# Kernel optimization log

Measured on AMD Instinct MI355X. Metric: run time of the kernel, lower is better.

Reference implementation:

```python
import jax, jax.numpy as jnp
import numpy as np

ATT_H = 256
DEC_H = 512
CTX = 1024  # 2 * encoder_hidden_size


def setup_inputs() -> dict:
    key = jax.random.key(0)
    ks = jax.random.split(key, 8)
    B, T = 32, 4096
    prev = jax.random.normal(ks[0], (B, 1, DEC_H), dtype=jnp.float32)
    enc = jax.random.normal(ks[1], (B, T, CTX), dtype=jnp.float32)
    # nn.Linear params: weight [out,in], bias [out]
    W_w = jax.random.normal(ks[2], (ATT_H, DEC_H), dtype=jnp.float32) / np.sqrt(DEC_H)
    W_b = jax.random.normal(ks[3], (ATT_H,), dtype=jnp.float32) * 0.01
    U_w = jax.random.normal(ks[4], (ATT_H, CTX), dtype=jnp.float32) / np.sqrt(CTX)
    U_b = jax.random.normal(ks[5], (ATT_H,), dtype=jnp.float32) * 0.01
    v = jax.random.uniform(ks[6], (ATT_H,), dtype=jnp.float32)
    return {
        "batch_size": B,
        "max_seq_len": T,
        "previous_decoder_hidden_state": prev,
        "encoder_final_hidden_layers": enc,
        "W_w": W_w, "W_b": W_b, "U_w": U_w, "U_b": U_b, "v": v,
    }


def reference(batch_size, max_seq_len, previous_decoder_hidden_state,
              encoder_final_hidden_layers, W_w, W_b, U_w, U_b, v):
    # tmp_1: [B,1,H] = W(prev); tmp_3: [B,T,H] = U(enc)
    tmp1 = jnp.einsum('bod,hd->boh', previous_decoder_hidden_state, W_w) + W_b
    tmp3 = jnp.einsum('btc,hc->bth', encoder_final_hidden_layers, U_w) + U_b
    # energy: [B,T] = relu(tmp1 + tmp3) . v
    energy = jnp.einsum('bth,h->bt', jax.nn.relu(tmp1 + tmp3), v)
    alpha = jax.nn.softmax(energy, axis=1)  # [B,T]
    # weighted sum over time -> context [B, 2E]
    c = jnp.einsum('bt,btc->bc', alpha, encoder_final_hidden_layers)
    return c
```

## Files before the change

kernel.cpp:

```cpp
#include <hip/hip_runtime.h>
#include <hip/hip_bf16.h>

#define BB   32
#define TT   4096
#define CTXD 1024
#define HH   256
#define DH   512
#define BT   64
#define NTILES (TT/BT)
#define BK   64
#define LDA  72

typedef __attribute__((ext_vector_type(8))) short bf16x8;
typedef __attribute__((ext_vector_type(4))) float f32x4;

static __device__ __forceinline__ unsigned short f2bf(float f) {
    unsigned int u = __float_as_uint(f);
    u += 0x7FFF + ((u >> 16) & 1);
    return (unsigned short)(u >> 16);
}

__global__ void uconv_kernel(const float* __restrict__ Uw, unsigned short* __restrict__ Ub) {
    int idx = blockIdx.x * blockDim.x + threadIdx.x;
    float4 u4 = ((const float4*)Uw)[idx];
    ushort4 o;
    o.x = f2bf(u4.x); o.y = f2bf(u4.y); o.z = f2bf(u4.z); o.w = f2bf(u4.w);
    ((ushort4*)Ub)[idx] = o;
}

__global__ void bias_kernel(const float* __restrict__ prev, const float* __restrict__ Ww,
                            const float* __restrict__ Wb, const float* __restrict__ Ubias,
                            float* __restrict__ bias) {
    __shared__ float ps[DH];
    int b = blockIdx.x, h = threadIdx.x;
    if (h < DH / 4) ((float4*)ps)[h] = ((const float4*)(prev + (size_t)b * DH))[h];
    __syncthreads();
    float acc = Wb[h] + Ubias[h];
    const float4* wr = (const float4*)(Ww + (size_t)h * DH);
    #pragma unroll 4
    for (int d = 0; d < DH / 4; ++d) {
        float4 w4 = wr[d];
        float4 p4 = ((const float4*)ps)[d];
        acc += w4.x * p4.x + w4.y * p4.y + w4.z * p4.z + w4.w * p4.w;
    }
    bias[b * HH + h] = acc;
}

__global__ void attn_main(const float* __restrict__ enc, const unsigned short* __restrict__ Ub,
                          const float* __restrict__ bias, const float* __restrict__ v,
                          float* __restrict__ partO, float* __restrict__ partM,
                          float* __restrict__ partL) {
    __shared__ __align__(16) unsigned short As[BT * LDA];
    __shared__ __align__(16) unsigned short Us[HH * LDA];
    __shared__ float epart[4][BT];
    __shared__ float pbuf[BT];

    const int tid  = threadIdx.x;
    const int lane = tid & 63;
    const int w    = tid >> 6;
    const int quad = lane >> 4;
    const int l15  = lane & 15;
    const int b    = blockIdx.x & 31;
    const int tile = blockIdx.x >> 5;
    const int t0   = tile * BT;
    const int pi   = b * NTILES + tile;

    const float* encBase = enc + ((size_t)b * TT + t0) * CTXD;

    f32x4 acc[4][4];
    #pragma unroll
    for (int mi = 0; mi < 4; ++mi)
        #pragma unroll
        for (int ni = 0; ni < 4; ++ni) acc[mi][ni] = (f32x4){0.f, 0.f, 0.f, 0.f};

    const int arow = tid >> 4;
    const int acg  = tid & 15;

    for (int kt = 0; kt < CTXD / BK; ++kt) {
        const float* ga = encBase + kt * BK;
        #pragma unroll
        for (int rr = 0; rr < 4; ++rr) {
            int row = arow + rr * 16;
            float4 a4 = *(const float4*)(ga + (size_t)row * CTXD + acg * 4);
            ushort4 o;
            o.x = f2bf(a4.x); o.y = f2bf(a4.y); o.z = f2bf(a4.z); o.w = f2bf(a4.w);
            *(ushort4*)&As[row * LDA + acg * 4] = o;
        }
        #pragma unroll
        for (int ii = 0; ii < 8; ++ii) {
            int idx = ii * 256 + tid;
            int row = idx >> 3;
            int g   = idx & 7;
            uint4 u = *(const uint4*)(Ub + (size_t)row * CTXD + kt * BK + g * 8);
            *(uint4*)&Us[row * LDA + g * 8] = u;
        }
        __syncthreads();
        #pragma unroll
        for (int ks = 0; ks < BK / 32; ++ks) {
            bf16x8 af[4], bfr[4];
            #pragma unroll
            for (int mi = 0; mi < 4; ++mi)
                af[mi] = *(const bf16x8*)&As[(mi * 16 + l15) * LDA + ks * 32 + quad * 8];
            #pragma unroll
            for (int ni = 0; ni < 4; ++ni)
                bfr[ni] = *(const bf16x8*)&Us[(w * 64 + ni * 16 + l15) * LDA + ks * 32 + quad * 8];
            #pragma unroll
            for (int mi = 0; mi < 4; ++mi)
                #pragma unroll
                for (int ni = 0; ni < 4; ++ni)
                    acc[mi][ni] = __builtin_amdgcn_mfma_f32_16x16x32_bf16(af[mi], bfr[ni], acc[mi][ni], 0, 0, 0);
        }
        __syncthreads();
    }

    float vv[4], bb[4];
    #pragma unroll
    for (int ni = 0; ni < 4; ++ni) {
        int h = w * 64 + ni * 16 + l15;
        vv[ni] = v[h];
        bb[ni] = bias[b * HH + h];
    }
    #pragma unroll
    for (int mi = 0; mi < 4; ++mi) {
        #pragma unroll
        for (int r = 0; r < 4; ++r) {
            float e = 0.f;
            #pragma unroll
            for (int ni = 0; ni < 4; ++ni) {
                float x = acc[mi][ni][r] + bb[ni];
                e += fmaxf(x, 0.f) * vv[ni];
            }
            e += __shfl_xor(e, 1);
            e += __shfl_xor(e, 2);
            e += __shfl_xor(e, 4);
            e += __shfl_xor(e, 8);
            if (l15 == 0) epart[w][mi * 16 + quad * 4 + r] = e;
        }
    }
    __syncthreads();

    if (tid < 64) {
        float e = epart[0][tid] + epart[1][tid] + epart[2][tid] + epart[3][tid];
        float m = e;
        #pragma unroll
        for (int off = 32; off; off >>= 1) m = fmaxf(m, __shfl_xor(m, off));
        float p = __expf(e - m);
        float l = p;
        #pragma unroll
        for (int off = 32; off; off >>= 1) l += __shfl_xor(l, off);
        pbuf[tid] = p;
        if (tid == 0) { partM[pi] = m; partL[pi] = l; }
    }
    __syncthreads();

    float4 o4 = {0.f, 0.f, 0.f, 0.f};
    #pragma unroll 4
    for (int t = 0; t < BT; ++t) {
        float p = pbuf[t];
        float4 ev = *(const float4*)(encBase + (size_t)t * CTXD + tid * 4);
        o4.x += p * ev.x; o4.y += p * ev.y; o4.z += p * ev.z; o4.w += p * ev.w;
    }
    *(float4*)(partO + (size_t)pi * CTXD + tid * 4) = o4;
}

__global__ void combine_kernel(const float* __restrict__ partO, const float* __restrict__ partM,
                               const float* __restrict__ partL, float* __restrict__ out) {
    __shared__ float sc[NTILES];
    __shared__ float sL;
    int b = blockIdx.x, tid = threadIdx.x;
    if (tid < 64) {
        float m = partM[b * NTILES + tid];
        float l = partL[b * NTILES + tid];
        float M = m;
        #pragma unroll
        for (int off = 32; off; off >>= 1) M = fmaxf(M, __shfl_xor(M, off));
        float s = __expf(m - M);
        sc[tid] = s;
        float Lp = l * s;
        #pragma unroll
        for (int off = 32; off; off >>= 1) Lp += __shfl_xor(Lp, off);
        if (tid == 0) sL = Lp;
    }
    __syncthreads();
    float4 o = {0.f, 0.f, 0.f, 0.f};
    const float* base = partO + (size_t)b * NTILES * CTXD;
    #pragma unroll 4
    for (int i = 0; i < NTILES; ++i) {
        float s = sc[i];
        float4 p4 = *(const float4*)(base + (size_t)i * CTXD + tid * 4);
        o.x += s * p4.x; o.y += s * p4.y; o.z += s * p4.z; o.w += s * p4.w;
    }
    float inv = 1.0f / sL;
    float4 r; r.x = o.x * inv; r.y = o.y * inv; r.z = o.z * inv; r.w = o.w * inv;
    ((float4*)out)[b * (CTXD / 4) + tid] = r;
}

extern "C" void kernel_launch(void* const* d_in, const int* in_sizes, int n_in,
                              void* d_out, int out_size, void* d_ws, size_t ws_size,
                              hipStream_t stream) {
    const float* prev  = (const float*)d_in[2];
    const float* enc   = (const float*)d_in[3];
    const float* Ww    = (const float*)d_in[4];
    const float* Wb    = (const float*)d_in[5];
    const float* Uw    = (const float*)d_in[6];
    const float* Ubias = (const float*)d_in[7];
    const float* v     = (const float*)d_in[8];
    float* out = (float*)d_out;

    char* ws = (char*)d_ws;
    float* bias          = (float*)ws;
    unsigned short* Ub   = (unsigned short*)(ws + 32768);
    float* partO         = (float*)(ws + 32768 + 524288);
    float* partM         = partO + (size_t)BB * NTILES * CTXD;
    float* partL         = partM + BB * NTILES;

    uconv_kernel<<<dim3(256), dim3(256), 0, stream>>>(Uw, Ub);
    bias_kernel<<<dim3(BB), dim3(HH), 0, stream>>>(prev, Ww, Wb, Ubias, bias);
    attn_main<<<dim3(BB * NTILES), dim3(256), 0, stream>>>(enc, Ub, bias, v, partO, partM, partL);
    combine_kernel<<<dim3(BB), dim3(256), 0, stream>>>(partO, partM, partL, out);
}
```

Baseline: 863.5 us.

## Double-buffer encoder tile in LDS and read U fragments directly from global

Double-buffers the bf16-converted encoder tile in shared memory and prefetches the next K-slice into registers while the MFMAs run on the current one, so each iteration needs only one barrier. The U weight tile is no longer staged in LDS; each wave loads its bf16 B fragments straight from global memory, relying on L2 and L1 because every block reads the same weights. This shrinks LDS use, which may raise occupancy, and drops the U staging traffic. The cost is uncoalesced strided global loads on the MFMA critical path.

New measurement: 877.2 us. About the same (+1.6%).

```diff
diff --git a/kernel.cpp b/kernel.cpp
--- a/kernel.cpp
+++ b/kernel.cpp
@@ -50,8 +50,7 @@
                           const float* __restrict__ bias, const float* __restrict__ v,
                           float* __restrict__ partO, float* __restrict__ partM,
                           float* __restrict__ partL) {
-    __shared__ __align__(16) unsigned short As[BT * LDA];
-    __shared__ __align__(16) unsigned short Us[HH * LDA];
+    __shared__ __align__(16) unsigned short As[2][BT * LDA];
     __shared__ float epart[4][BT];
     __shared__ float pbuf[BT];
 
@@ -66,6 +65,7 @@
     const int pi   = b * NTILES + tile;
 
     const float* encBase = enc + ((size_t)b * TT + t0) * CTXD;
+    const unsigned short* ubase = Ub + (size_t)(w * 64) * CTXD;
 
     f32x4 acc[4][4];
     #pragma unroll
@@ -76,39 +76,51 @@
     const int arow = tid >> 4;
     const int acg  = tid & 15;
 
-    for (int kt = 0; kt < CTXD / BK; ++kt) {
-        const float* ga = encBase + kt * BK;
+    {
         #pragma unroll
         for (int rr = 0; rr < 4; ++rr) {
             int row = arow + rr * 16;
-            float4 a4 = *(const float4*)(ga + (size_t)row * CTXD + acg * 4);
+            float4 a4 = *(const float4*)(encBase + (size_t)row * CTXD + acg * 4);
             ushort4 o;
             o.x = f2bf(a4.x); o.y = f2bf(a4.y); o.z = f2bf(a4.z); o.w = f2bf(a4.w);
-            *(ushort4*)&As[row * LDA + acg * 4] = o;
-        }
-        #pragma unroll
-        for (int ii = 0; ii < 8; ++ii) {
-            int idx = ii * 256 + tid;
-            int row = idx >> 3;
-            int g   = idx & 7;
-            uint4 u = *(const uint4*)(Ub + (size_t)row * CTXD + kt * BK + g * 8);
-            *(uint4*)&Us[row * LDA + g * 8] = u;
-        }
-        __syncthreads();
+            *(ushort4*)&As[0][row * LDA + acg * 4] = o;
+        }
+    }
+    __syncthreads();
+
+    float4 pre[4];
+    for (int kt = 0; kt < CTXD / BK; ++kt) {
+        const int cur = kt & 1;
+        if (kt < CTXD / BK - 1) {
+            const float* gn = encBase + (kt + 1) * BK;
+            #pragma unroll
+            for (int rr = 0; rr < 4; ++rr)
+                pre[rr] = *(const float4*)(gn + (size_t)(arow + rr * 16) * CTXD + acg * 4);
+        }
         #pragma unroll
         for (int ks = 0; ks < BK / 32; ++ks) {
             bf16x8 af[4], bfr[4];
             #pragma unroll
             for (int mi = 0; mi < 4; ++mi)
-                af[mi] = *(const bf16x8*)&As[(mi * 16 + l15) * LDA + ks * 32 + quad * 8];
+                af[mi] = *(const bf16x8*)&As[cur][(mi * 16 + l15) * LDA + ks * 32 + quad * 8];
             #pragma unroll
             for (int ni = 0; ni < 4; ++ni)
-                bfr[ni] = *(const bf16x8*)&Us[(w * 64 + ni * 16 + l15) * LDA + ks * 32 + quad * 8];
+                bfr[ni] = *(const bf16x8*)(ubase + (size_t)(ni * 16 + l15) * CTXD + kt * BK + ks * 32 + quad * 8);
             #pragma unroll
             for (int mi = 0; mi < 4; ++mi)
                 #pragma unroll
                 for (int ni = 0; ni < 4; ++ni)
                     acc[mi][ni] = __builtin_amdgcn_mfma_f32_16x16x32_bf16(af[mi], bfr[ni], acc[mi][ni], 0, 0, 0);
+        }
+        if (kt < CTXD / BK - 1) {
+            #pragma unroll
+            for (int rr = 0; rr < 4; ++rr) {
+                int row = arow + rr * 16;
+                ushort4 o;
+                o.x = f2bf(pre[rr].x); o.y = f2bf(pre[rr].y);
+                o.z = f2bf(pre[rr].z); o.w = f2bf(pre[rr].w);
+                *(ushort4*)&As[cur ^ 1][row * LDA + acg * 4] = o;
+            }
         }
         __syncthreads();
     }
```
